# Optimization experiments

Hardware: AMD Instinct MI355X
Metric: run time of the kernel (lower is better)

## Reference

```python
import jax, jax.numpy as jnp
import numpy as np


def setup_inputs() -> dict:
    key = jax.random.key(0)
    k1, k2 = jax.random.split(key)
    y = jax.random.normal(k1, (2048, 256), dtype=jnp.float32)  # (num_labels, 2*hidden)
    x = jax.random.normal(k2, (1024, 128), dtype=jnp.float32)  # (batch, hidden)
    return {"y": y, "x": x}


def reference(y, x):
    h = y.shape[-1] // 2
    # box parameters: min coordinate and softplus delta
    mn = y[:, :h][None, :, :]                      # (1, L, h)
    delta = jax.nn.softplus(y[:, h:])[None, :, :]  # (1, L, h)
    mx = mn + delta
    center = mn + delta / 2.0
    dp1 = delta + 1.0
    xr = x[:, None, :]                             # (B, 1, h)
    l1 = jnp.abs(xr - center)                      # (B, L, h)
    inside = (mn <= xr) & (xr <= mx)
    outside_dist = l1 * dp1 - delta / 2.0 * (delta - 1.0 / (delta + 1e-10))
    per_dim = jnp.where(inside, l1 / (dp1 + 1e-10), outside_dist)
    distance = jnp.linalg.norm(per_dim, axis=-1)   # (B, L)
    return -distance
```

## Files before the change

kernel.cpp:

```cpp
#include <hip/hip_runtime.h>
#include <hip/hip_bf16.h>
#include <math.h>


#define BM 32
#define BN 64
#define TM 8

__global__ void boxe_prep(const float* __restrict__ y, const float* __restrict__ x,
                          float4* __restrict__ p4, float* __restrict__ xT)
{
    int idx = blockIdx.x * blockDim.x + threadIdx.x;
    if (idx < 2048 * 128) {
        int n = idx & 2047;
        int k = idx >> 11;
        float mn = y[n * 256 + k];
        float dv = y[n * 256 + 128 + k];
        float delta = fmaxf(dv, 0.0f) + log1pf(expf(-fabsf(dv)));
        float hd = 0.5f * delta;
        float center = mn + hd;
        float dp1 = delta + 1.0f;
        float inv = 1.0f / (dp1 + 1e-10f);
        float cc = hd * (delta - 1.0f / (delta + 1e-10f));
        p4[idx] = make_float4(center, hd, inv, cc);
    } else {
        int j = idx - 2048 * 128;
        if (j < 1024 * 128) {
            int m = j & 1023;
            int k = j >> 10;
            xT[j] = x[m * 128 + k];
        }
    }
}

__global__ __launch_bounds__(256) void boxe_main(
    const float4* __restrict__ p4, const float* __restrict__ xT,
    float* __restrict__ out)
{
    __shared__ float xtile[128][BM];

    const int tid  = threadIdx.x;
    const int lane = tid & 63;
    const int wave = tid >> 6;
    const int m0   = blockIdx.y * BM;
    const int n0   = blockIdx.x * BN;

#pragma unroll
    for (int i = 0; i < (128 * BM) / 256; ++i) {
        int idx = i * 256 + tid;
        int k = idx >> 5;
        int m = idx & (BM - 1);
        xtile[k][m] = xT[k * 1024 + m0 + m];
    }
    __syncthreads();

    float acc[TM];
#pragma unroll
    for (int r = 0; r < TM; ++r) acc[r] = 0.0f;

    const int n  = n0 + lane;
    const int mw = wave * TM;

#pragma unroll 4
    for (int k = 0; k < 128; ++k) {
        float4 p = p4[k * 2048 + n];
        float dp1 = fmaf(2.0f, p.y, 1.0f);
#pragma unroll
        for (int r = 0; r < TM; ++r) {
            float xv = xtile[k][mw + r];
            float l = fabsf(xv - p.x);
            float v = (l <= p.y) ? (l * p.z) : fmaf(l, dp1, -p.w);
            acc[r] = fmaf(v, v, acc[r]);
        }
    }

#pragma unroll
    for (int r = 0; r < TM; ++r) {
        int m = m0 + mw + r;
        out[m * 2048 + n] = -sqrtf(acc[r]);
    }
}

extern "C" void kernel_launch(void* const* d_in, const int* in_sizes, int n_in,
                              void* d_out, int out_size, void* d_ws, size_t ws_size,
                              hipStream_t stream) {
    const float* y = (const float*)d_in[0];
    const float* x = (const float*)d_in[1];
    float* out = (float*)d_out;

    char* ws = (char*)d_ws;
    float4* p4 = (float4*)ws;
    float*  xT = (float*)(ws + 4u * 1024 * 1024);

    int total = 2048 * 128 + 1024 * 128;
    hipLaunchKernelGGL(boxe_prep, dim3(total / 256), dim3(256), 0, stream,
                       y, x, p4, xT);

    dim3 grid(2048 / BN, 1024 / BM);
    hipLaunchKernelGGL(boxe_main, grid, dim3(256), 0, stream,
                       p4, xT, out);
}
```

Before: 117.9 us.

## Coalesce prep via shared-memory transpose and drop separate x transpose pass

The prep kernel now reads y rows coalesced, computes the box parameters, and transposes them through padded shared memory so that the float4 writes stay coalesced. The separate global transpose of x is removed: the main kernel loads x rows directly and transposes them into a padded shared tile. This removes strided global accesses and an extra workspace round trip. The inner k-loop unroll is also raised from 4 to 8, which may increase register pressure.

```diff
diff --git a/kernel.cpp b/kernel.cpp
--- a/kernel.cpp
+++ b/kernel.cpp
@@ -7,37 +7,45 @@
 #define BN 64
 #define TM 8
 
-__global__ void boxe_prep(const float* __restrict__ y, const float* __restrict__ x,
-                          float4* __restrict__ p4, float* __restrict__ xT)
+__global__ __launch_bounds__(256) void boxe_prep(const float* __restrict__ y,
+                                                 float4* __restrict__ p4)
 {
-    int idx = blockIdx.x * blockDim.x + threadIdx.x;
-    if (idx < 2048 * 128) {
-        int n = idx & 2047;
-        int k = idx >> 11;
+    __shared__ float t0[128][9], t1[128][9], t2[128][9], t3[128][9];
+    const int tid = threadIdx.x;
+    const int n0  = blockIdx.x * 8;
+
+#pragma unroll
+    for (int i = 0; i < 4; ++i) {
+        int j  = i * 256 + tid;
+        int k  = j & 127;
+        int nl = j >> 7;
+        int n  = n0 + nl;
         float mn = y[n * 256 + k];
         float dv = y[n * 256 + 128 + k];
         float delta = fmaxf(dv, 0.0f) + log1pf(expf(-fabsf(dv)));
-        float hd = 0.5f * delta;
-        float center = mn + hd;
-        float dp1 = delta + 1.0f;
-        float inv = 1.0f / (dp1 + 1e-10f);
-        float cc = hd * (delta - 1.0f / (delta + 1e-10f));
-        p4[idx] = make_float4(center, hd, inv, cc);
-    } else {
-        int j = idx - 2048 * 128;
-        if (j < 1024 * 128) {
-            int m = j & 1023;
-            int k = j >> 10;
-            xT[j] = x[m * 128 + k];
-        }
+        float hd  = 0.5f * delta;
+        t0[k][nl] = mn + hd;
+        t1[k][nl] = hd;
+        t2[k][nl] = 1.0f / (delta + 1.0f + 1e-10f);
+        t3[k][nl] = hd * (delta - 1.0f / (delta + 1e-10f));
+    }
+    __syncthreads();
+
+#pragma unroll
+    for (int i = 0; i < 4; ++i) {
+        int j  = i * 256 + tid;
+        int nl = j & 7;
+        int k  = j >> 3;
+        p4[k * 2048 + n0 + nl] =
+            make_float4(t0[k][nl], t1[k][nl], t2[k][nl], t3[k][nl]);
     }
 }
 
 __global__ __launch_bounds__(256) void boxe_main(
-    const float4* __restrict__ p4, const float* __restrict__ xT,
+    const float4* __restrict__ p4, const float* __restrict__ x,
     float* __restrict__ out)
 {
-    __shared__ float xtile[128][BM];
+    __shared__ float xtile[128][BM + 1];
 
     const int tid  = threadIdx.x;
     const int lane = tid & 63;
@@ -48,9 +56,9 @@
 #pragma unroll
     for (int i = 0; i < (128 * BM) / 256; ++i) {
         int idx = i * 256 + tid;
-        int k = idx >> 5;
-        int m = idx & (BM - 1);
-        xtile[k][m] = xT[k * 1024 + m0 + m];
+        int m = idx >> 7;
+        int k = idx & 127;
+        xtile[k][m] = x[(m0 + m) * 128 + k];
     }
     __syncthreads();
 
@@ -61,7 +69,7 @@
     const int n  = n0 + lane;
     const int mw = wave * TM;
 
-#pragma unroll 4
+#pragma unroll 8
     for (int k = 0; k < 128; ++k) {
         float4 p = p4[k * 2048 + n];
         float dp1 = fmaf(2.0f, p.y, 1.0f);
@@ -88,15 +96,10 @@
     const float* x = (const float*)d_in[1];
     float* out = (float*)d_out;
 
-    char* ws = (char*)d_ws;
-    float4* p4 = (float4*)ws;
-    float*  xT = (float*)(ws + 4u * 1024 * 1024);
+    float4* p4 = (float4*)d_ws;
 
-    int total = 2048 * 128 + 1024 * 128;
-    hipLaunchKernelGGL(boxe_prep, dim3(total / 256), dim3(256), 0, stream,
-                       y, x, p4, xT);
+    hipLaunchKernelGGL(boxe_prep, dim3(2048 / 8), dim3(256), 0, stream, y, p4);
 
     dim3 grid(2048 / BN, 1024 / BM);
-    hipLaunchKernelGGL(boxe_main, grid, dim3(256), 0, stream,
-                       p4, xT, out);
+    hipLaunchKernelGGL(boxe_main, grid, dim3(256), 0, stream, p4, x, out);
 }
```

Result: no change. 118.1 us (+0.1%).
